# Kernel tuning notes

Hardware: AMD Instinct MI355X
Metric: run time of the kernel (lower is better)

Reference implementation:

```python
import jax, jax.numpy as jnp
import numpy as np
from jax import lax

B_J0 = 0.01   # config.b_j0
R_M = 1.0     # config.R_m
BETA = 1.8    # isAdapt=1 branch
GAMMA = 0.5   # config.gamma
LENS = 0.5    # config.lens
SCALE = 6.0   # config.scale
HIGHT = 0.15  # config.hight


def _gauss(x, mu, sigma):
    return jnp.exp(-(x - mu) ** 2 / (2.0 * sigma ** 2)) / jnp.sqrt(2.0 * jnp.pi) / sigma


@jax.custom_vjp
def spike_fn(x):
    return (x > 0).astype(x.dtype)

def _spike_fwd(x):
    return spike_fn(x), x

def _spike_bwd(x, g):
    # 'MG' multi-gaussian surrogate gradient from ActFun_adp.backward
    temp = (_gauss(x, 0.0, LENS) * (1.0 + HIGHT)
            - _gauss(x, LENS, SCALE * LENS) * HIGHT
            - _gauss(x, -LENS, SCALE * LENS) * HIGHT)
    return (g * temp * GAMMA,)

spike_fn.defvjp(_spike_fwd, _spike_bwd)


def setup_inputs() -> dict:
    key = jax.random.key(0)
    ks = jax.random.split(key, 20)
    B, T, I, H, O = 256, 250, 700, 128, 20
    def xav(k, shape):
        lim = jnp.sqrt(6.0 / (shape[0] + shape[1]))
        return jax.random.uniform(k, shape, jnp.float32, -lim, lim)
    def orth(k, n):
        a = jax.random.normal(k, (n, n), jnp.float32)
        q, r = jnp.linalg.qr(a)
        return q * jnp.sign(jnp.diag(r))[None, :]
    return {
        'input': jax.random.normal(ks[0], (B, T, I), jnp.float32),
        'A1_mask': jnp.ones((H, H), jnp.float32),
        'A2_mask': jnp.ones((H, H), jnp.float32),
        'W_ih1': xav(ks[1], (H, I)), 'b_ih1': jnp.zeros((H,), jnp.float32),
        'W_h1h1': orth(ks[2], H), 'b_h1h1': jnp.zeros((H,), jnp.float32),
        'W_h1h2': xav(ks[3], (H, H)), 'b_h1h2': jnp.zeros((H,), jnp.float32),
        'W_h2h2': orth(ks[4], H), 'b_h2h2': jnp.zeros((H,), jnp.float32),
        'W_h2o': xav(ks[5], (O, H)), 'b_h2o': jnp.zeros((O,), jnp.float32),
        'tau_adp_h1': 150.0 + 10.0 * jax.random.normal(ks[6], (H,), jnp.float32),
        'tau_adp_h2': 150.0 + 10.0 * jax.random.normal(ks[7], (H,), jnp.float32),
        'tau_m_h1': 20.0 + 5.0 * jax.random.normal(ks[8], (H,), jnp.float32),
        'tau_m_h2': 20.0 + 5.0 * jax.random.normal(ks[9], (H,), jnp.float32),
        'tau_m_o': 20.0 + 5.0 * jax.random.normal(ks[10], (O,), jnp.float32),
        'hid1_mem0': jax.random.uniform(ks[11], (B, H), jnp.float32),
        'hid2_mem0': jax.random.uniform(ks[12], (B, H), jnp.float32),
        'out_mem0': jax.random.uniform(ks[13], (B, O), jnp.float32),
    }


def reference(input, A1_mask, A2_mask,
              W_ih1, b_ih1, W_h1h1, b_h1h1, W_h1h2, b_h1h2,
              W_h2h2, b_h2h2, W_h2o, b_h2o,
              tau_adp_h1, tau_adp_h2, tau_m_h1, tau_m_h2, tau_m_o,
              hid1_mem0, hid2_mem0, out_mem0):
    B, T, _ = input.shape
    H = W_ih1.shape[0]
    O = W_h2o.shape[0]
    # time-constant decays (dt = 1), computed once
    a1 = jnp.exp(-1.0 / tau_m_h1)
    r1 = jnp.exp(-1.0 / tau_adp_h1)
    a2 = jnp.exp(-1.0 / tau_m_h2)
    r2 = jnp.exp(-1.0 / tau_adp_h2)
    ao = jnp.exp(-1.0 / tau_m_o)

    xT = jnp.swapaxes(input, 0, 1)  # [T, B, I]
    carry0 = (hid1_mem0, jnp.zeros((B, H), input.dtype), jnp.full((B, H), B_J0, input.dtype),
              hid2_mem0, jnp.zeros((B, H), input.dtype), jnp.full((B, H), B_J0, input.dtype),
              out_mem0, jnp.zeros((B, O), input.dtype))

    def step(carry, xs):
        x_t, t = xs
        h1m, h1s, b1, h2m, h2s, b2, om, acc = carry
        # layer 1: input + recurrent drive, adaptive threshold LIF update
        in1 = x_t @ W_ih1.T + b_ih1 + h1s @ W_h1h1.T + b_h1h1
        b1 = r1 * b1 + (1.0 - r1) * h1s
        Bth1 = B_J0 + BETA * b1
        h1m = h1m * a1 + (1.0 - a1) * R_M * in1 - Bth1 * h1s
        h1s = spike_fn(h1m - Bth1)
        # layer 2
        in2 = h1s @ W_h1h2.T + b_h1h2 + h2s @ W_h2h2.T + b_h2h2
        b2 = r2 * b2 + (1.0 - r2) * h2s
        Bth2 = B_J0 + BETA * b2
        h2m = h2m * a2 + (1.0 - a2) * R_M * in2 - Bth2 * h2s
        h2s = spike_fn(h2m - Bth2)
        # leaky-integrator readout (no spike)
        om = om * ao + (1.0 - ao) * R_M * (h2s @ W_h2o.T + b_h2o)
        # accumulate softmax only for t > 10
        acc = acc + jnp.where(t > 10, 1.0, 0.0) * jax.nn.softmax(om, axis=1)
        return (h1m, h1s, b1, h2m, h2s, b2, om, acc), None

    final, _ = lax.scan(step, carry0, (xT, jnp.arange(T)))
    output = final[-1]
    A_norm = jnp.sum(jnp.abs(W_h1h1)) + jnp.sum(jnp.abs(W_h2h2))
    return output, A_norm


if __name__ == '__main__':
    out = reference(**setup_inputs())
    print(out[0].shape, out[1])
```

## Files before the change

kernel.cpp:

```cpp
#include <hip/hip_runtime.h>
#include <hip/hip_bf16.h>
#include <stdint.h>

#define HN 128
#define TSTEPS 250
#define ON 20
#define GK 700
#define NKT 22

typedef _Float16 h2 __attribute__((ext_vector_type(2)));
typedef _Float16 h8 __attribute__((ext_vector_type(8)));
typedef float f4 __attribute__((ext_vector_type(4)));

__device__ __forceinline__ uint32_t pack2u(float x, float y) {
    h2 p; p.x = (_Float16)x; p.y = (_Float16)y;
    return __builtin_bit_cast(uint32_t, p);
}

__global__ __launch_bounds__(256) void ff_gemm(const float* __restrict__ X,
                                               const float* __restrict__ W,
                                               const float* __restrict__ bias,
                                               float* __restrict__ out) {
    __shared__ __align__(16) uint32_t Xs[2][128][16];
    __shared__ __align__(16) uint32_t Ws[2][128][16];
    const int tid   = threadIdx.x;
    const int w     = tid >> 6;
    const int lane  = tid & 63;
    const int m0    = blockIdx.x * 128;
    const int srow  = tid & 127;
    const int shalf = tid >> 7;
    const int lr    = lane & 15;
    const int lg    = lane >> 4;

    f4 acc[2][8];
#pragma unroll
    for (int m = 0; m < 2; ++m)
#pragma unroll
        for (int n = 0; n < 8; ++n) acc[m][n] = (f4){0.f, 0.f, 0.f, 0.f};

    float4 x4[4], w4[4];

#define LOADT(t)                                                               \
    {                                                                          \
        const int k0 = (t) * 32 + shalf * 16;                                  \
        if ((t) < 21 || shalf == 0) {                                          \
            _Pragma("unroll")                                                  \
            for (int q = 0; q < 4; ++q) {                                      \
                x4[q] = *(const float4*)&X[(size_t)(m0 + srow) * GK + k0 + q * 4]; \
                w4[q] = *(const float4*)&W[(size_t)srow * GK + k0 + q * 4];    \
            }                                                                  \
        } else {                                                               \
            _Pragma("unroll")                                                  \
            for (int q = 0; q < 3; ++q) {                                      \
                x4[q] = *(const float4*)&X[(size_t)(m0 + srow) * GK + k0 + q * 4]; \
                w4[q] = *(const float4*)&W[(size_t)srow * GK + k0 + q * 4];    \
            }                                                                  \
            x4[3] = (float4){0.f, 0.f, 0.f, 0.f};                              \
            w4[3] = (float4){0.f, 0.f, 0.f, 0.f};                              \
        }                                                                      \
    }
#define STORET(buf)                                                            \
    {                                                                          \
        _Pragma("unroll")                                                      \
        for (int q = 0; q < 4; ++q) {                                          \
            Xs[buf][srow][shalf * 8 + 2 * q]     = pack2u(x4[q].x, x4[q].y);   \
            Xs[buf][srow][shalf * 8 + 2 * q + 1] = pack2u(x4[q].z, x4[q].w);   \
            Ws[buf][srow][shalf * 8 + 2 * q]     = pack2u(w4[q].x, w4[q].y);   \
            Ws[buf][srow][shalf * 8 + 2 * q + 1] = pack2u(w4[q].z, w4[q].w);   \
        }                                                                      \
    }

    LOADT(0);
    STORET(0);
    __syncthreads();
    int cur = 0;
    for (int t = 0; t < NKT; ++t) {
        if (t + 1 < NKT) LOADT(t + 1);
        h8 a[2];
#pragma unroll
        for (int m = 0; m < 2; ++m) {
            const uint4 au = *(const uint4*)&Xs[cur][w * 32 + m * 16 + lr][lg * 4];
            a[m] = __builtin_bit_cast(h8, au);
        }
#pragma unroll
        for (int n = 0; n < 8; ++n) {
            const uint4 bu = *(const uint4*)&Ws[cur][n * 16 + lr][lg * 4];
            const h8 bf = __builtin_bit_cast(h8, bu);
            acc[0][n] = __builtin_amdgcn_mfma_f32_16x16x32_f16(a[0], bf, acc[0][n], 0, 0, 0);
            acc[1][n] = __builtin_amdgcn_mfma_f32_16x16x32_f16(a[1], bf, acc[1][n], 0, 0, 0);
        }
        if (t + 1 < NKT) STORET(cur ^ 1);
        __syncthreads();
        cur ^= 1;
    }

    float bv[8];
#pragma unroll
    for (int n = 0; n < 8; ++n) bv[n] = bias[n * 16 + lr];
#pragma unroll
    for (int m = 0; m < 2; ++m)
#pragma unroll
        for (int q = 0; q < 4; ++q) {
            const size_t row = (size_t)(m0 + w * 32 + m * 16 + lg * 4 + q);
#pragma unroll
            for (int n = 0; n < 8; ++n)
                out[row * HN + n * 16 + lr] = acc[m][n][q] + bv[n];
        }
#undef LOADT
#undef STORET
}

__device__ __forceinline__ void qrow(const float* __restrict__ src,
                                     uint4 (&wq)[8], float& sc) {
    float amax = 0.f;
#pragma unroll
    for (int q = 0; q < 32; ++q) {
        float4 v = *(const float4*)&src[q * 4];
        amax = fmaxf(amax, fmaxf(fmaxf(fabsf(v.x), fabsf(v.y)),
                                 fmaxf(fabsf(v.z), fabsf(v.w))));
    }
    const float qs = (amax > 0.f) ? 127.f / amax : 0.f;
#pragma unroll
    for (int g = 0; g < 8; ++g) {
        uint32_t u[4];
#pragma unroll
        for (int e = 0; e < 4; ++e) {
            float4 v = *(const float4*)&src[g * 16 + e * 4];
            const int q0 = (int)rintf(v.x * qs), q1 = (int)rintf(v.y * qs);
            const int q2 = (int)rintf(v.z * qs), q3 = (int)rintf(v.w * qs);
            u[e] = (uint32_t)(q0 & 255) | ((uint32_t)(q1 & 255) << 8) |
                   ((uint32_t)(q2 & 255) << 16) | ((uint32_t)(q3 & 255) << 24);
        }
        wq[g].x = u[0]; wq[g].y = u[1]; wq[g].z = u[2]; wq[g].w = u[3];
    }
    sc = (amax > 0.f) ? amax / 127.f : 0.f;
}

__device__ __forceinline__ int mvqr(const uint4 (&wq)[8], const uint4 (&sv)[8]) {
    int a0 = 0, a1 = 0, a2 = 0, a3 = 0;
#pragma unroll
    for (int g = 0; g < 8; ++g) {
        a0 = __builtin_amdgcn_sdot4((int)wq[g].x, (int)sv[g].x, a0, false);
        a1 = __builtin_amdgcn_sdot4((int)wq[g].y, (int)sv[g].y, a1, false);
        a2 = __builtin_amdgcn_sdot4((int)wq[g].z, (int)sv[g].z, a2, false);
        a3 = __builtin_amdgcn_sdot4((int)wq[g].w, (int)sv[g].w, a3, false);
    }
    return (a0 + a1) + (a2 + a3);
}

#define LOADQ(arr, buf, sv)                                                    \
    {                                                                          \
        const uint4* _p = (const uint4*)&arr[buf][0];                          \
        _Pragma("unroll") for (int _g = 0; _g < 8; ++_g) sv[_g] = _p[_g];      \
    }

__device__ __forceinline__ uint32_t nib2bytes(uint32_t nib) {
    return ((nib & 15u) * 0x00204081u) & 0x01010101u;
}

__device__ __forceinline__ void spread_masks(unsigned long long lo,
                                             unsigned long long hi,
                                             uint4 (&sv)[8]) {
#pragma unroll
    for (int g = 0; g < 8; ++g) {
        const unsigned long long src = (g < 4) ? lo : hi;
        const int base = (g & 3) * 16;
        sv[g].x = nib2bytes((uint32_t)(src >> (base + 0)));
        sv[g].y = nib2bytes((uint32_t)(src >> (base + 4)));
        sv[g].z = nib2bytes((uint32_t)(src >> (base + 8)));
        sv[g].w = nib2bytes((uint32_t)(src >> (base + 12)));
    }
}

#define LDS_FENCE() asm volatile("s_waitcnt lgkmcnt(0)" ::: "memory")

#define PROG_S1 0
#define PROG_B  1
#define PROG_C  2
#define PROG_RO 3
#define PROG_OM 4

__global__ __launch_bounds__(320) void srnn_pipe12(
    const float* __restrict__ ff,
    const float* __restrict__ W_h1h1, const float* __restrict__ b_h1h1,
    const float* __restrict__ W_h1h2, const float* __restrict__ b_h1h2,
    const float* __restrict__ W_h2h2, const float* __restrict__ b_h2h2,
    const float* __restrict__ W_h2o,  const float* __restrict__ b_h2o,
    const float* __restrict__ tau_adp_h1, const float* __restrict__ tau_adp_h2,
    const float* __restrict__ tau_m_h1,   const float* __restrict__ tau_m_h2,
    const float* __restrict__ tau_m_o,
    const float* __restrict__ h1m0, const float* __restrict__ h2m0,
    const float* __restrict__ om0,
    float* __restrict__ out) {
    const int b    = blockIdx.x;
    const int tid  = threadIdx.x;
    const int w    = tid >> 6;
    const int lane = tid & 63;

    __shared__ __align__(16) uint32_t s1ring[8][32];
    __shared__ __align__(16) uint32_t s2ring[8][32];
    __shared__ __align__(16) float    pBring[8][HN];
    __shared__ __align__(16) float    rdring[8][32];
    __shared__ int prog[8];

    if (tid < 8) prog[tid] = 0;
    __syncthreads();

#define WAIT_GE(idx, target, cache)                                            \
    if ((cache) < (target)) {                                                  \
        volatile int* _p = (volatile int*)&prog[idx];                          \
        int _v = *_p;                                                          \
        while (_v < (target)) _v = *_p;                                        \
        (cache) = _v;                                                          \
        LDS_FENCE();                                                           \
    }
#define PUBLISH(idx, val)                                                      \
    {                                                                          \
        LDS_FENCE();                                                           \
        if (lane == 0) ((volatile int*)prog)[idx] = (val);                     \
    }

    if (w == 0) {
        const int jl = lane, jh = lane + 64;
        uint4 wql[8], wqh[8]; float sAl, sAh;
        qrow(W_h1h1 + jl * HN, wql, sAl);
        qrow(W_h1h1 + jh * HN, wqh, sAh);
        float h1m_l = h1m0[b * HN + jl], h1m_h = h1m0[b * HN + jh];
        const float a1l = expf(-1.f / tau_m_h1[jl]), a1h = expf(-1.f / tau_m_h1[jh]);
        const float r1l = expf(-1.f / tau_adp_h1[jl]), r1h = expf(-1.f / tau_adp_h1[jh]);
        const float bil = b_h1h1[jl], bih = b_h1h1[jh];
        float b1l = 0.01f, b1h = 0.01f, s1l = 0.f, s1h = 0.f;
        const float* fpl = ff + (size_t)b * TSTEPS * HN + jl;
        const float* fph = ff + (size_t)b * TSTEPS * HN + jh;
        float fcl = fpl[0], fnl = fpl[HN];
        float fch = fph[0], fnh = fph[HN];
        unsigned long long mklo = 0ull, mkhi = 0ull;
        int cB = 0;
        for (int t = 0; t < TSTEPS; ++t) {
            const float f2l = (t + 2 < TSTEPS) ? fpl[(size_t)(t + 2) * HN] : 0.f;
            const float f2h = (t + 2 < TSTEPS) ? fph[(size_t)(t + 2) * HN] : 0.f;
            uint4 sv[8];
            spread_masks(mklo, mkhi, sv);
            const float pAl = sAl * (float)mvqr(wql, sv);
            const float pAh = sAh * (float)mvqr(wqh, sv);
            b1l = r1l * b1l + (1.f - r1l) * s1l;
            b1h = r1h * b1h + (1.f - r1h) * s1h;
            const float Btl = 0.01f + 1.8f * b1l;
            const float Bth = 0.01f + 1.8f * b1h;
            h1m_l = h1m_l * a1l + (1.f - a1l) * (fcl + bil + pAl) - Btl * s1l;
            h1m_h = h1m_h * a1h + (1.f - a1h) * (fch + bih + pAh) - Bth * s1h;
            const int spl = (h1m_l - Btl > 0.f) ? 1 : 0;
            const int sph = (h1m_h - Bth > 0.f) ? 1 : 0;
            s1l = (float)spl; s1h = (float)sph;
            mklo = __ballot(spl); mkhi = __ballot(sph);
            WAIT_GE(PROG_B, t - 7, cB);
            if (lane < 32) {
                const unsigned long long src = (lane < 16) ? mklo : mkhi;
                s1ring[t & 7][lane] = nib2bytes((uint32_t)(src >> ((lane & 15) * 4)));
            }
            PUBLISH(PROG_S1, t + 1);
            fcl = fnl; fnl = f2l; fch = fnh; fnh = f2h;
        }
    } else if (w == 1) {
        const int jl = lane, jh = lane + 64;
        uint4 wql[8], wqh[8]; float sBl, sBh;
        qrow(W_h1h2 + jl * HN, wql, sBl);
        qrow(W_h1h2 + jh * HN, wqh, sBh);
        int cS1 = 0, cC = 0;
        for (int t = 0; t < TSTEPS; ++t) {
            WAIT_GE(PROG_S1, t + 1, cS1);
            uint4 sv[8];
            LOADQ(s1ring, t & 7, sv);
            const float pl = sBl * (float)mvqr(wql, sv);
            const float ph = sBh * (float)mvqr(wqh, sv);
            WAIT_GE(PROG_C, t - 7, cC);
            pBring[t & 7][jl] = pl;
            pBring[t & 7][jh] = ph;
            PUBLISH(PROG_B, t + 1);
        }
    } else if (w == 2) {
        const int jl = lane, jh = lane + 64;
        uint4 wql[8], wqh[8]; float sCl, sCh;
        qrow(W_h2h2 + jl * HN, wql, sCl);
        qrow(W_h2h2 + jh * HN, wqh, sCh);
        float h2m_l = h2m0[b * HN + jl], h2m_h = h2m0[b * HN + jh];
        const float a2l = expf(-1.f / tau_m_h2[jl]), a2h = expf(-1.f / tau_m_h2[jh]);
        const float r2l = expf(-1.f / tau_adp_h2[jl]), r2h = expf(-1.f / tau_adp_h2[jh]);
        const float bil = b_h1h2[jl] + b_h2h2[jl];
        const float bih = b_h1h2[jh] + b_h2h2[jh];
        float b2l = 0.01f, b2h = 0.01f, s2l = 0.f, s2h = 0.f;
        unsigned long long mklo = 0ull, mkhi = 0ull;
        int cB = 0, cRO = 0;
        for (int t = 0; t < TSTEPS; ++t) {
            uint4 sv[8];
            spread_masks(mklo, mkhi, sv);
            const float pCl = sCl * (float)mvqr(wql, sv);
            const float pCh = sCh * (float)mvqr(wqh, sv);
            WAIT_GE(PROG_B, t + 1, cB);
            const float pBl = pBring[t & 7][jl];
            const float pBh = pBring[t & 7][jh];
            b2l = r2l * b2l + (1.f - r2l) * s2l;
            b2h = r2h * b2h + (1.f - r2h) * s2h;
            const float Btl = 0.01f + 1.8f * b2l;
            const float Bth = 0.01f + 1.8f * b2h;
            h2m_l = h2m_l * a2l + (1.f - a2l) * (pBl + pCl + bil) - Btl * s2l;
            h2m_h = h2m_h * a2h + (1.f - a2h) * (pBh + pCh + bih) - Bth * s2h;
            const int spl = (h2m_l - Btl > 0.f) ? 1 : 0;
            const int sph = (h2m_h - Bth > 0.f) ? 1 : 0;
            s2l = (float)spl; s2h = (float)sph;
            mklo = __ballot(spl); mkhi = __ballot(sph);
            WAIT_GE(PROG_RO, t - 7, cRO);
            if (lane < 32) {
                const unsigned long long src = (lane < 16) ? mklo : mkhi;
                s2ring[t & 7][lane] = nib2bytes((uint32_t)(src >> ((lane & 15) * 4)));
            }
            PUBLISH(PROG_C, t + 1);
        }
    } else if (w == 3) {
        const int o = lane;
        uint4 wq[8]; float sO;
        qrow(W_h2o + (size_t)((o < ON) ? o : 0) * HN, wq, sO);
        if (o >= ON) sO = 0.f;
        int cC = 0, cOM = 0;
        for (int t = 0; t < TSTEPS; ++t) {
            WAIT_GE(PROG_C, t + 1, cC);
            uint4 sv[8];
            LOADQ(s2ring, t & 7, sv);
            const float r = sO * (float)mvqr(wq, sv);
            WAIT_GE(PROG_OM, t - 7, cOM);
            if (o < 32) rdring[t & 7][o] = (o < ON) ? r : 0.f;
            PUBLISH(PROG_RO, t + 1);
        }
    } else {
        float omv[ON], accv[ON], aov[ON], bov[ON];
#pragma unroll
        for (int k = 0; k < ON; ++k) {
            omv[k]  = om0[b * ON + k];
            aov[k]  = expf(-1.f / tau_m_o[k]);
            bov[k]  = b_h2o[k];
            accv[k] = 0.f;
        }
        int cRO = 0;
        for (int t = 0; t < TSTEPS; ++t) {
            WAIT_GE(PROG_RO, t + 1, cRO);
            const float4* rp = (const float4*)&rdring[t & 7][0];
            const float4 r0 = rp[0], r1 = rp[1], r2 = rp[2], r3 = rp[3], r4 = rp[4];
            float rd[ON];
            rd[0] = r0.x;  rd[1] = r0.y;  rd[2] = r0.z;  rd[3] = r0.w;
            rd[4] = r1.x;  rd[5] = r1.y;  rd[6] = r1.z;  rd[7] = r1.w;
            rd[8] = r2.x;  rd[9] = r2.y;  rd[10] = r2.z; rd[11] = r2.w;
            rd[12] = r3.x; rd[13] = r3.y; rd[14] = r3.z; rd[15] = r3.w;
            rd[16] = r4.x; rd[17] = r4.y; rd[18] = r4.z; rd[19] = r4.w;
            PUBLISH(PROG_OM, t + 1);
#pragma unroll
            for (int k = 0; k < ON; ++k)
                omv[k] = omv[k] * aov[k] + (1.f - aov[k]) * (rd[k] + bov[k]);
            float m0 = omv[0], m1 = omv[1], m2 = omv[2], m3 = omv[3];
#pragma unroll
            for (int k = 4; k < ON; k += 4) {
                m0 = fmaxf(m0, omv[k]);
                m1 = fmaxf(m1, omv[k + 1]);
                m2 = fmaxf(m2, omv[k + 2]);
                m3 = fmaxf(m3, omv[k + 3]);
            }
            const float mx = fmaxf(fmaxf(m0, m1), fmaxf(m2, m3));
            float e[ON];
            float d0 = 0.f, d1 = 0.f, d2 = 0.f, d3 = 0.f;
#pragma unroll
            for (int k = 0; k < ON; k += 4) {
                e[k]     = __expf(omv[k] - mx);     d0 += e[k];
                e[k + 1] = __expf(omv[k + 1] - mx); d1 += e[k + 1];
                e[k + 2] = __expf(omv[k + 2] - mx); d2 += e[k + 2];
                e[k + 3] = __expf(omv[k + 3] - mx); d3 += e[k + 3];
            }
            const float den = (d0 + d1) + (d2 + d3);
            if (t > 10) {
                const float rden = 1.f / den;
#pragma unroll
                for (int k = 0; k < ON; ++k)
                    accv[k] = fmaf(e[k], rden, accv[k]);
            }
        }
        if (lane == 0) {
#pragma unroll
            for (int k = 0; k < ON; ++k) out[b * ON + k] = accv[k];
        }
    }
#undef WAIT_GE
#undef PUBLISH
}

__global__ void anorm_kernel(const float* __restrict__ W1,
                             const float* __restrict__ W2,
                             float* __restrict__ out) {
    __shared__ float red[256];
    float s = 0.f;
    for (int i = threadIdx.x; i < HN * HN; i += 256)
        s += fabsf(W1[i]) + fabsf(W2[i]);
    red[threadIdx.x] = s;
    __syncthreads();
    for (int off = 128; off > 0; off >>= 1) {
        if (threadIdx.x < off) red[threadIdx.x] += red[threadIdx.x + off];
        __syncthreads();
    }
    if (threadIdx.x == 0) out[256 * ON] = red[0];
}

extern "C" void kernel_launch(void* const* d_in, const int* in_sizes, int n_in,
                              void* d_out, int out_size, void* d_ws, size_t ws_size,
                              hipStream_t stream) {
    const float* input      = (const float*)d_in[0];
    const float* W_ih1      = (const float*)d_in[3];
    const float* b_ih1      = (const float*)d_in[4];
    const float* W_h1h1     = (const float*)d_in[5];
    const float* b_h1h1     = (const float*)d_in[6];
    const float* W_h1h2     = (const float*)d_in[7];
    const float* b_h1h2     = (const float*)d_in[8];
    const float* W_h2h2     = (const float*)d_in[9];
    const float* b_h2h2     = (const float*)d_in[10];
    const float* W_h2o      = (const float*)d_in[11];
    const float* b_h2o      = (const float*)d_in[12];
    const float* tau_adp_h1 = (const float*)d_in[13];
    const float* tau_adp_h2 = (const float*)d_in[14];
    const float* tau_m_h1   = (const float*)d_in[15];
    const float* tau_m_h2   = (const float*)d_in[16];
    const float* tau_m_o    = (const float*)d_in[17];
    const float* h1m0       = (const float*)d_in[18];
    const float* h2m0       = (const float*)d_in[19];
    const float* om0        = (const float*)d_in[20];

    float* out   = (float*)d_out;
    float* ffbuf = (float*)d_ws;

    anorm_kernel<<<1, 256, 0, stream>>>(W_h1h1, W_h2h2, out);
    ff_gemm<<<500, 256, 0, stream>>>(input, W_ih1, b_ih1, ffbuf);
    srnn_pipe12<<<256, 320, 0, stream>>>(ffbuf, W_h1h1, b_h1h1, W_h1h2, b_h1h2,
                                         W_h2h2, b_h2h2, W_h2o, b_h2o,
                                         tau_adp_h1, tau_adp_h2,
                                         tau_m_h1, tau_m_h2, tau_m_o,
                                         h1m0, h2m0, om0, out);
}
```

Baseline: 239.2 us.

## Replace per-step LDS spin-wait flags with chunked barrier-synchronized wavefront pipeline

```diff
diff --git a/kernel.cpp b/kernel.cpp
--- a/kernel.cpp
+++ b/kernel.cpp
@@ -7,6 +7,8 @@
 #define ON 20
 #define GK 700
 #define NKT 22
+#define KS 4
+#define NSLOT 63
 
 typedef _Float16 h2 __attribute__((ext_vector_type(2)));
 typedef _Float16 h8 __attribute__((ext_vector_type(8)));
@@ -148,9 +150,9 @@
     return (a0 + a1) + (a2 + a3);
 }
 
-#define LOADQ(arr, buf, sv)                                                    \
+#define LOADQP(ptr, sv)                                                        \
     {                                                                          \
-        const uint4* _p = (const uint4*)&arr[buf][0];                          \
+        const uint4* _p = (const uint4*)(ptr);                                 \
         _Pragma("unroll") for (int _g = 0; _g < 8; ++_g) sv[_g] = _p[_g];      \
     }
 
@@ -172,15 +174,7 @@
     }
 }
 
-#define LDS_FENCE() asm volatile("s_waitcnt lgkmcnt(0)" ::: "memory")
-
-#define PROG_S1 0
-#define PROG_B  1
-#define PROG_C  2
-#define PROG_RO 3
-#define PROG_OM 4
-
-__global__ __launch_bounds__(320) void srnn_pipe12(
+__global__ __launch_bounds__(320) void srnn_pipe13(
     const float* __restrict__ ff,
     const float* __restrict__ W_h1h1, const float* __restrict__ b_h1h1,
     const float* __restrict__ W_h1h2, const float* __restrict__ b_h1h2,
@@ -197,28 +191,10 @@
     const int w    = tid >> 6;
     const int lane = tid & 63;
 
-    __shared__ __align__(16) uint32_t s1ring[8][32];
-    __shared__ __align__(16) uint32_t s2ring[8][32];
-    __shared__ __align__(16) float    pBring[8][HN];
-    __shared__ __align__(16) float    rdring[8][32];
-    __shared__ int prog[8];
-
-    if (tid < 8) prog[tid] = 0;
-    __syncthreads();
-
-#define WAIT_GE(idx, target, cache)                                            \
-    if ((cache) < (target)) {                                                  \
-        volatile int* _p = (volatile int*)&prog[idx];                          \
-        int _v = *_p;                                                          \
-        while (_v < (target)) _v = *_p;                                        \
-        (cache) = _v;                                                          \
-        LDS_FENCE();                                                           \
-    }
-#define PUBLISH(idx, val)                                                      \
-    {                                                                          \
-        LDS_FENCE();                                                           \
-        if (lane == 0) ((volatile int*)prog)[idx] = (val);                     \
-    }
+    __shared__ __align__(16) uint32_t s1buf[2][KS][32];
+    __shared__ __align__(16) uint32_t s2buf[2][KS][32];
+    __shared__ __align__(16) float    pbbuf[2][KS][HN];
+    __shared__ __align__(16) float    rdbuf[2][KS][32];
 
     if (w == 0) {
         const int jl = lane, jh = lane + 64;
@@ -232,51 +208,71 @@
         float b1l = 0.01f, b1h = 0.01f, s1l = 0.f, s1h = 0.f;
         const float* fpl = ff + (size_t)b * TSTEPS * HN + jl;
         const float* fph = ff + (size_t)b * TSTEPS * HN + jh;
-        float fcl = fpl[0], fnl = fpl[HN];
-        float fch = fph[0], fnh = fph[HN];
+        float fcl[KS], fch[KS];
+#pragma unroll
+        for (int k = 0; k < KS; ++k) {
+            fcl[k] = fpl[(size_t)k * HN];
+            fch[k] = fph[(size_t)k * HN];
+        }
         unsigned long long mklo = 0ull, mkhi = 0ull;
-        int cB = 0;
-        for (int t = 0; t < TSTEPS; ++t) {
-            const float f2l = (t + 2 < TSTEPS) ? fpl[(size_t)(t + 2) * HN] : 0.f;
-            const float f2h = (t + 2 < TSTEPS) ? fph[(size_t)(t + 2) * HN] : 0.f;
-            uint4 sv[8];
-            spread_masks(mklo, mkhi, sv);
-            const float pAl = sAl * (float)mvqr(wql, sv);
-            const float pAh = sAh * (float)mvqr(wqh, sv);
-            b1l = r1l * b1l + (1.f - r1l) * s1l;
-            b1h = r1h * b1h + (1.f - r1h) * s1h;
-            const float Btl = 0.01f + 1.8f * b1l;
-            const float Bth = 0.01f + 1.8f * b1h;
-            h1m_l = h1m_l * a1l + (1.f - a1l) * (fcl + bil + pAl) - Btl * s1l;
-            h1m_h = h1m_h * a1h + (1.f - a1h) * (fch + bih + pAh) - Bth * s1h;
-            const int spl = (h1m_l - Btl > 0.f) ? 1 : 0;
-            const int sph = (h1m_h - Bth > 0.f) ? 1 : 0;
-            s1l = (float)spl; s1h = (float)sph;
-            mklo = __ballot(spl); mkhi = __ballot(sph);
-            WAIT_GE(PROG_B, t - 7, cB);
-            if (lane < 32) {
-                const unsigned long long src = (lane < 16) ? mklo : mkhi;
-                s1ring[t & 7][lane] = nib2bytes((uint32_t)(src >> ((lane & 15) * 4)));
-            }
-            PUBLISH(PROG_S1, t + 1);
-            fcl = fnl; fnl = f2l; fch = fnh; fnh = f2h;
+        for (int s = 0; s < NSLOT + 4; ++s) {
+            float fnl[KS], fnh[KS];
+#pragma unroll
+            for (int k = 0; k < KS; ++k) {
+                const int t = KS * (s + 1) + k;
+                fnl[k] = (t < TSTEPS) ? fpl[(size_t)t * HN] : 0.f;
+                fnh[k] = (t < TSTEPS) ? fph[(size_t)t * HN] : 0.f;
+            }
+            if (s < NSLOT) {
+#pragma unroll
+                for (int k = 0; k < KS; ++k) {
+                    const int t = KS * s + k;
+                    if (t < TSTEPS) {
+                        uint4 sv[8];
+                        spread_masks(mklo, mkhi, sv);
+                        const float pAl = sAl * (float)mvqr(wql, sv);
+                        const float pAh = sAh * (float)mvqr(wqh, sv);
+                        b1l = r1l * b1l + (1.f - r1l) * s1l;
+                        b1h = r1h * b1h + (1.f - r1h) * s1h;
+                        const float Btl = 0.01f + 1.8f * b1l;
+                        const float Bth = 0.01f + 1.8f * b1h;
+                        h1m_l = h1m_l * a1l + (1.f - a1l) * (fcl[k] + bil + pAl) - Btl * s1l;
+                        h1m_h = h1m_h * a1h + (1.f - a1h) * (fch[k] + bih + pAh) - Bth * s1h;
+                        const int spl = (h1m_l - Btl > 0.f) ? 1 : 0;
+                        const int sph = (h1m_h - Bth > 0.f) ? 1 : 0;
+                        s1l = (float)spl; s1h = (float)sph;
+                        mklo = __ballot(spl); mkhi = __ballot(sph);
+                        if (lane < 32) {
+                            const unsigned long long src = (lane < 16) ? mklo : mkhi;
+                            s1buf[s & 1][k][lane] =
+                                nib2bytes((uint32_t)(src >> ((lane & 15) * 4)));
+                        }
+                    }
+                }
+            }
+#pragma unroll
+            for (int k = 0; k < KS; ++k) { fcl[k] = fnl[k]; fch[k] = fnh[k]; }
+            __syncthreads();
         }
     } else if (w == 1) {
         const int jl = lane, jh = lane + 64;
         uint4 wql[8], wqh[8]; float sBl, sBh;
         qrow(W_h1h2 + jl * HN, wql, sBl);
         qrow(W_h1h2 + jh * HN, wqh, sBh);
-        int cS1 = 0, cC = 0;
-        for (int t = 0; t < TSTEPS; ++t) {
-            WAIT_GE(PROG_S1, t + 1, cS1);
-            uint4 sv[8];
-            LOADQ(s1ring, t & 7, sv);
-            const float pl = sBl * (float)mvqr(wql, sv);
-            const float ph = sBh * (float)mvqr(wqh, sv);
-            WAIT_GE(PROG_C, t - 7, cC);
-            pBring[t & 7][jl] = pl;
-            pBring[t & 7][jh] = ph;
-            PUBLISH(PROG_B, t + 1);
+        for (int s = 0; s < NSLOT + 4; ++s) {
+            if (s >= 1 && s - 1 < NSLOT) {
+#pragma unroll
+                for (int k = 0; k < KS; ++k) {
+                    const int t = KS * (s - 1) + k;
+                    if (t < TSTEPS) {
+                        uint4 sv[8];
+                        LOADQP(&s1buf[(s - 1) & 1][k][0], sv);
+                        pbbuf[s & 1][k][jl] = sBl * (float)mvqr(wql, sv);
+                        pbbuf[s & 1][k][jh] = sBh * (float)mvqr(wqh, sv);
+                    }
+                }
+            }
+            __syncthreads();
         }
     } else if (w == 2) {
         const int jl = lane, jh = lane + 64;
@@ -290,46 +286,56 @@
         const float bih = b_h1h2[jh] + b_h2h2[jh];
         float b2l = 0.01f, b2h = 0.01f, s2l = 0.f, s2h = 0.f;
         unsigned long long mklo = 0ull, mkhi = 0ull;
-        int cB = 0, cRO = 0;
-        for (int t = 0; t < TSTEPS; ++t) {
-            uint4 sv[8];
-            spread_masks(mklo, mkhi, sv);
-            const float pCl = sCl * (float)mvqr(wql, sv);
-            const float pCh = sCh * (float)mvqr(wqh, sv);
-            WAIT_GE(PROG_B, t + 1, cB);
-            const float pBl = pBring[t & 7][jl];
-            const float pBh = pBring[t & 7][jh];
-            b2l = r2l * b2l + (1.f - r2l) * s2l;
-            b2h = r2h * b2h + (1.f - r2h) * s2h;
-            const float Btl = 0.01f + 1.8f * b2l;
-            const float Bth = 0.01f + 1.8f * b2h;
-            h2m_l = h2m_l * a2l + (1.f - a2l) * (pBl + pCl + bil) - Btl * s2l;
-            h2m_h = h2m_h * a2h + (1.f - a2h) * (pBh + pCh + bih) - Bth * s2h;
-            const int spl = (h2m_l - Btl > 0.f) ? 1 : 0;
-            const int sph = (h2m_h - Bth > 0.f) ? 1 : 0;
-            s2l = (float)spl; s2h = (float)sph;
-            mklo = __ballot(spl); mkhi = __ballot(sph);
-            WAIT_GE(PROG_RO, t - 7, cRO);
-            if (lane < 32) {
-                const unsigned long long src = (lane < 16) ? mklo : mkhi;
-                s2ring[t & 7][lane] = nib2bytes((uint32_t)(src >> ((lane & 15) * 4)));
-            }
-            PUBLISH(PROG_C, t + 1);
+        for (int s = 0; s < NSLOT + 4; ++s) {
+            if (s >= 2 && s - 2 < NSLOT) {
+#pragma unroll
+                for (int k = 0; k < KS; ++k) {
+                    const int t = KS * (s - 2) + k;
+                    if (t < TSTEPS) {
+                        uint4 sv[8];
+                        spread_masks(mklo, mkhi, sv);
+                        const float pCl = sCl * (float)mvqr(wql, sv);
+                        const float pCh = sCh * (float)mvqr(wqh, sv);
+                        const float pBl = pbbuf[(s - 1) & 1][k][jl];
+                        const float pBh = pbbuf[(s - 1) & 1][k][jh];
+                        b2l = r2l * b2l + (1.f - r2l) * s2l;
+                        b2h = r2h * b2h + (1.f - r2h) * s2h;
+                        const float Btl = 0.01f + 1.8f * b2l;
+                        const float Bth = 0.01f + 1.8f * b2h;
+                        h2m_l = h2m_l * a2l + (1.f - a2l) * (pBl + pCl + bil) - Btl * s2l;
+                        h2m_h = h2m_h * a2h + (1.f - a2h) * (pBh + pCh + bih) - Bth * s2h;
+                        const int spl = (h2m_l - Btl > 0.f) ? 1 : 0;
+                        const int sph = (h2m_h - Bth > 0.f) ? 1 : 0;
+                        s2l = (float)spl; s2h = (float)sph;
+                        mklo = __ballot(spl); mkhi = __ballot(sph);
+                        if (lane < 32) {
+                            const unsigned long long src = (lane < 16) ? mklo : mkhi;
+                            s2buf[s & 1][k][lane] =
+                                nib2bytes((uint32_t)(src >> ((lane & 15) * 4)));
+                        }
+                    }
+                }
+            }
+            __syncthreads();
         }
     } else if (w == 3) {
         const int o = lane;
         uint4 wq[8]; float sO;
         qrow(W_h2o + (size_t)((o < ON) ? o : 0) * HN, wq, sO);
         if (o >= ON) sO = 0.f;
-        int cC = 0, cOM = 0;
-        for (int t = 0; t < TSTEPS; ++t) {
-            WAIT_GE(PROG_C, t + 1, cC);
-            uint4 sv[8];
-            LOADQ(s2ring, t & 7, sv);
-            const float r = sO * (float)mvqr(wq, sv);
-            WAIT_GE(PROG_OM, t - 7, cOM);
-            if (o < 32) rdring[t & 7][o] = (o < ON) ? r : 0.f;
-            PUBLISH(PROG_RO, t + 1);
+        for (int s = 0; s < NSLOT + 4; ++s) {
+            if (s >= 3 && s - 3 < NSLOT) {
+#pragma unroll
+                for (int k = 0; k < KS; ++k) {
+                    const int t = KS * (s - 3) + k;
+                    if (t < TSTEPS) {
+                        uint4 sv[8];
+                        LOADQP(&s2buf[(s - 1) & 1][k][0], sv);
+                        if (o < 32) rdbuf[s & 1][k][o] = sO * (float)mvqr(wq, sv);
+                    }
+                }
+            }
+            __syncthreads();
         }
     } else {
         float omv[ON], accv[ON], aov[ON], bov[ON];
@@ -340,54 +346,59 @@
             bov[k]  = b_h2o[k];
             accv[k] = 0.f;
         }
-        int cRO = 0;
-        for (int t = 0; t < TSTEPS; ++t) {
-            WAIT_GE(PROG_RO, t + 1, cRO);
-            const float4* rp = (const float4*)&rdring[t & 7][0];
-            const float4 r0 = rp[0], r1 = rp[1], r2 = rp[2], r3 = rp[3], r4 = rp[4];
-            float rd[ON];
-            rd[0] = r0.x;  rd[1] = r0.y;  rd[2] = r0.z;  rd[3] = r0.w;
-            rd[4] = r1.x;  rd[5] = r1.y;  rd[6] = r1.z;  rd[7] = r1.w;
-            rd[8] = r2.x;  rd[9] = r2.y;  rd[10] = r2.z; rd[11] = r2.w;
-            rd[12] = r3.x; rd[13] = r3.y; rd[14] = r3.z; rd[15] = r3.w;
-            rd[16] = r4.x; rd[17] = r4.y; rd[18] = r4.z; rd[19] = r4.w;
-            PUBLISH(PROG_OM, t + 1);
-#pragma unroll
-            for (int k = 0; k < ON; ++k)
-                omv[k] = omv[k] * aov[k] + (1.f - aov[k]) * (rd[k] + bov[k]);
-            float m0 = omv[0], m1 = omv[1], m2 = omv[2], m3 = omv[3];
-#pragma unroll
-            for (int k = 4; k < ON; k += 4) {
-                m0 = fmaxf(m0, omv[k]);
-                m1 = fmaxf(m1, omv[k + 1]);
-                m2 = fmaxf(m2, omv[k + 2]);
-                m3 = fmaxf(m3, omv[k + 3]);
-            }
-            const float mx = fmaxf(fmaxf(m0, m1), fmaxf(m2, m3));
-            float e[ON];
-            float d0 = 0.f, d1 = 0.f, d2 = 0.f, d3 = 0.f;
-#pragma unroll
-            for (int k = 0; k < ON; k += 4) {
-                e[k]     = __expf(omv[k] - mx);     d0 += e[k];
-                e[k + 1] = __expf(omv[k + 1] - mx); d1 += e[k + 1];
-                e[k + 2] = __expf(omv[k + 2] - mx); d2 += e[k + 2];
-                e[k + 3] = __expf(omv[k + 3] - mx); d3 += e[k + 3];
-            }
-            const float den = (d0 + d1) + (d2 + d3);
-            if (t > 10) {
-                const float rden = 1.f / den;
-#pragma unroll
-                for (int k = 0; k < ON; ++k)
-                    accv[k] = fmaf(e[k], rden, accv[k]);
-            }
+        for (int s = 0; s < NSLOT + 4; ++s) {
+            if (s >= 4 && s - 4 < NSLOT) {
+#pragma unroll
+                for (int kk = 0; kk < KS; ++kk) {
+                    const int t = KS * (s - 4) + kk;
+                    if (t < TSTEPS) {
+                        const float4* rp = (const float4*)&rdbuf[(s - 1) & 1][kk][0];
+                        const float4 r0 = rp[0], r1 = rp[1], r2 = rp[2],
+                                     r3 = rp[3], r4 = rp[4];
+                        float rd[ON];
+                        rd[0] = r0.x;  rd[1] = r0.y;  rd[2] = r0.z;  rd[3] = r0.w;
+                        rd[4] = r1.x;  rd[5] = r1.y;  rd[6] = r1.z;  rd[7] = r1.w;
+                        rd[8] = r2.x;  rd[9] = r2.y;  rd[10] = r2.z; rd[11] = r2.w;
+                        rd[12] = r3.x; rd[13] = r3.y; rd[14] = r3.z; rd[15] = r3.w;
+                        rd[16] = r4.x; rd[17] = r4.y; rd[18] = r4.z; rd[19] = r4.w;
+#pragma unroll
+                        for (int k = 0; k < ON; ++k)
+                            omv[k] = omv[k] * aov[k] + (1.f - aov[k]) * (rd[k] + bov[k]);
+                        float m0 = omv[0], m1 = omv[1], m2 = omv[2], m3 = omv[3];
+#pragma unroll
+                        for (int k = 4; k < ON; k += 4) {
+                            m0 = fmaxf(m0, omv[k]);
+                            m1 = fmaxf(m1, omv[k + 1]);
+                            m2 = fmaxf(m2, omv[k + 2]);
+                            m3 = fmaxf(m3, omv[k + 3]);
+                        }
+                        const float mx = fmaxf(fmaxf(m0, m1), fmaxf(m2, m3));
+                        float e[ON];
+                        float d0 = 0.f, d1 = 0.f, d2 = 0.f, d3 = 0.f;
+#pragma unroll
+                        for (int k = 0; k < ON; k += 4) {
+                            e[k]     = __expf(omv[k] - mx);     d0 += e[k];
+                            e[k + 1] = __expf(omv[k + 1] - mx); d1 += e[k + 1];
+                            e[k + 2] = __expf(omv[k + 2] - mx); d2 += e[k + 2];
+                            e[k + 3] = __expf(omv[k + 3] - mx); d3 += e[k + 3];
+                        }
+                        const float den = (d0 + d1) + (d2 + d3);
+                        if (t > 10) {
+                            const float rden = 1.f / den;
+#pragma unroll
+                            for (int k = 0; k < ON; ++k)
+                                accv[k] = fmaf(e[k], rden, accv[k]);
+                        }
+                    }
+                }
+            }
+            __syncthreads();
         }
         if (lane == 0) {
 #pragma unroll
             for (int k = 0; k < ON; ++k) out[b * ON + k] = accv[k];
         }
     }
-#undef WAIT_GE
-#undef PUBLISH
 }
 
 __global__ void anorm_kernel(const float* __restrict__ W1,
@@ -434,7 +445,7 @@
 
     anorm_kernel<<<1, 256, 0, stream>>>(W_h1h1, W_h2h2, out);
     ff_gemm<<<500, 256, 0, stream>>>(input, W_ih1, b_ih1, ffbuf);
-    srnn_pipe12<<<256, 320, 0, stream>>>(ffbuf, W_h1h1, b_h1h1, W_h1h2, b_h1h2,
+    srnn_pipe13<<<256, 320, 0, stream>>>(ffbuf, W_h1h1, b_h1h1, W_h1h2, b_h1h2,
                                          W_h2h2, b_h2h2, W_h2o, b_h2o,
                                          tau_adp_h1, tau_adp_h2,
                                          tau_m_h1, tau_m_h2, tau_m_o,
```

New measurement: 247.1 us. 1.03x slower.

## Collapse five-wave pipelined SRNN kernel into single-wave monolithic recurrence

Applied to the files above, without the earlier changes.

```diff
diff --git a/kernel.cpp b/kernel.cpp
--- a/kernel.cpp
+++ b/kernel.cpp
@@ -110,8 +110,13 @@
 #undef STORET
 }
 
-__device__ __forceinline__ void qrow(const float* __restrict__ src,
-                                     uint4 (&wq)[8], float& sc) {
+__device__ __forceinline__ float rlane(float v, int k) {
+    return __int_as_float(__builtin_amdgcn_readlane(__float_as_int(v), k));
+}
+
+template <int STRIDE>
+__device__ __forceinline__ void qrow_lds(const float* __restrict__ src,
+                                         uint4 (*WQ)[STRIDE], int j, float& sc) {
     float amax = 0.f;
 #pragma unroll
     for (int q = 0; q < 32; ++q) {
@@ -131,28 +136,26 @@
             u[e] = (uint32_t)(q0 & 255) | ((uint32_t)(q1 & 255) << 8) |
                    ((uint32_t)(q2 & 255) << 16) | ((uint32_t)(q3 & 255) << 24);
         }
-        wq[g].x = u[0]; wq[g].y = u[1]; wq[g].z = u[2]; wq[g].w = u[3];
+        uint4 w4; w4.x = u[0]; w4.y = u[1]; w4.z = u[2]; w4.w = u[3];
+        WQ[g][j] = w4;
     }
     sc = (amax > 0.f) ? amax / 127.f : 0.f;
 }
 
-__device__ __forceinline__ int mvqr(const uint4 (&wq)[8], const uint4 (&sv)[8]) {
+template <int STRIDE>
+__device__ __forceinline__ int mvql(const uint4 (*W)[STRIDE],
+                                    const uint4 (&sv)[8], int j) {
     int a0 = 0, a1 = 0, a2 = 0, a3 = 0;
 #pragma unroll
     for (int g = 0; g < 8; ++g) {
-        a0 = __builtin_amdgcn_sdot4((int)wq[g].x, (int)sv[g].x, a0, false);
-        a1 = __builtin_amdgcn_sdot4((int)wq[g].y, (int)sv[g].y, a1, false);
-        a2 = __builtin_amdgcn_sdot4((int)wq[g].z, (int)sv[g].z, a2, false);
-        a3 = __builtin_amdgcn_sdot4((int)wq[g].w, (int)sv[g].w, a3, false);
+        const uint4 wq = W[g][j];
+        a0 = __builtin_amdgcn_sdot4((int)wq.x, (int)sv[g].x, a0, false);
+        a1 = __builtin_amdgcn_sdot4((int)wq.y, (int)sv[g].y, a1, false);
+        a2 = __builtin_amdgcn_sdot4((int)wq.z, (int)sv[g].z, a2, false);
+        a3 = __builtin_amdgcn_sdot4((int)wq.w, (int)sv[g].w, a3, false);
     }
     return (a0 + a1) + (a2 + a3);
 }
-
-#define LOADQ(arr, buf, sv)                                                    \
-    {                                                                          \
-        const uint4* _p = (const uint4*)&arr[buf][0];                          \
-        _Pragma("unroll") for (int _g = 0; _g < 8; ++_g) sv[_g] = _p[_g];      \
-    }
 
 __device__ __forceinline__ uint32_t nib2bytes(uint32_t nib) {
     return ((nib & 15u) * 0x00204081u) & 0x01010101u;
@@ -172,15 +175,7 @@
     }
 }
 
-#define LDS_FENCE() asm volatile("s_waitcnt lgkmcnt(0)" ::: "memory")
-
-#define PROG_S1 0
-#define PROG_B  1
-#define PROG_C  2
-#define PROG_RO 3
-#define PROG_OM 4
-
-__global__ __launch_bounds__(320) void srnn_pipe12(
+__global__ __launch_bounds__(64) void srnn_mono(
     const float* __restrict__ ff,
     const float* __restrict__ W_h1h1, const float* __restrict__ b_h1h1,
     const float* __restrict__ W_h1h2, const float* __restrict__ b_h1h2,
@@ -193,201 +188,115 @@
     const float* __restrict__ om0,
     float* __restrict__ out) {
     const int b    = blockIdx.x;
-    const int tid  = threadIdx.x;
-    const int w    = tid >> 6;
-    const int lane = tid & 63;
-
-    __shared__ __align__(16) uint32_t s1ring[8][32];
-    __shared__ __align__(16) uint32_t s2ring[8][32];
-    __shared__ __align__(16) float    pBring[8][HN];
-    __shared__ __align__(16) float    rdring[8][32];
-    __shared__ int prog[8];
-
-    if (tid < 8) prog[tid] = 0;
+    const int lane = threadIdx.x;
+    const int jl = lane, jh = lane + 64;
+
+    __shared__ __align__(16) uint4 WQA[8][HN];
+    __shared__ __align__(16) uint4 WQB[8][HN];
+    __shared__ __align__(16) uint4 WQC[8][HN];
+    __shared__ __align__(16) uint4 WQO[8][64];
+
+    float sAl, sAh, sBl, sBh, sCl, sCh, sO;
+    qrow_lds<HN>(W_h1h1 + jl * HN, WQA, jl, sAl);
+    qrow_lds<HN>(W_h1h1 + jh * HN, WQA, jh, sAh);
+    qrow_lds<HN>(W_h1h2 + jl * HN, WQB, jl, sBl);
+    qrow_lds<HN>(W_h1h2 + jh * HN, WQB, jh, sBh);
+    qrow_lds<HN>(W_h2h2 + jl * HN, WQC, jl, sCl);
+    qrow_lds<HN>(W_h2h2 + jh * HN, WQC, jh, sCh);
+    qrow_lds<64>(W_h2o + (size_t)((lane < ON) ? lane : 0) * HN, WQO, lane, sO);
+    if (lane >= ON) sO = 0.f;
     __syncthreads();
 
-#define WAIT_GE(idx, target, cache)                                            \
-    if ((cache) < (target)) {                                                  \
-        volatile int* _p = (volatile int*)&prog[idx];                          \
-        int _v = *_p;                                                          \
-        while (_v < (target)) _v = *_p;                                        \
-        (cache) = _v;                                                          \
-        LDS_FENCE();                                                           \
-    }
-#define PUBLISH(idx, val)                                                      \
-    {                                                                          \
-        LDS_FENCE();                                                           \
-        if (lane == 0) ((volatile int*)prog)[idx] = (val);                     \
-    }
-
-    if (w == 0) {
-        const int jl = lane, jh = lane + 64;
-        uint4 wql[8], wqh[8]; float sAl, sAh;
-        qrow(W_h1h1 + jl * HN, wql, sAl);
-        qrow(W_h1h1 + jh * HN, wqh, sAh);
-        float h1m_l = h1m0[b * HN + jl], h1m_h = h1m0[b * HN + jh];
-        const float a1l = expf(-1.f / tau_m_h1[jl]), a1h = expf(-1.f / tau_m_h1[jh]);
-        const float r1l = expf(-1.f / tau_adp_h1[jl]), r1h = expf(-1.f / tau_adp_h1[jh]);
-        const float bil = b_h1h1[jl], bih = b_h1h1[jh];
-        float b1l = 0.01f, b1h = 0.01f, s1l = 0.f, s1h = 0.f;
-        const float* fpl = ff + (size_t)b * TSTEPS * HN + jl;
-        const float* fph = ff + (size_t)b * TSTEPS * HN + jh;
-        float fcl = fpl[0], fnl = fpl[HN];
-        float fch = fph[0], fnh = fph[HN];
-        unsigned long long mklo = 0ull, mkhi = 0ull;
-        int cB = 0;
-        for (int t = 0; t < TSTEPS; ++t) {
-            const float f2l = (t + 2 < TSTEPS) ? fpl[(size_t)(t + 2) * HN] : 0.f;
-            const float f2h = (t + 2 < TSTEPS) ? fph[(size_t)(t + 2) * HN] : 0.f;
-            uint4 sv[8];
-            spread_masks(mklo, mkhi, sv);
-            const float pAl = sAl * (float)mvqr(wql, sv);
-            const float pAh = sAh * (float)mvqr(wqh, sv);
-            b1l = r1l * b1l + (1.f - r1l) * s1l;
-            b1h = r1h * b1h + (1.f - r1h) * s1h;
-            const float Btl = 0.01f + 1.8f * b1l;
-            const float Bth = 0.01f + 1.8f * b1h;
-            h1m_l = h1m_l * a1l + (1.f - a1l) * (fcl + bil + pAl) - Btl * s1l;
-            h1m_h = h1m_h * a1h + (1.f - a1h) * (fch + bih + pAh) - Bth * s1h;
-            const int spl = (h1m_l - Btl > 0.f) ? 1 : 0;
-            const int sph = (h1m_h - Bth > 0.f) ? 1 : 0;
-            s1l = (float)spl; s1h = (float)sph;
-            mklo = __ballot(spl); mkhi = __ballot(sph);
-            WAIT_GE(PROG_B, t - 7, cB);
-            if (lane < 32) {
-                const unsigned long long src = (lane < 16) ? mklo : mkhi;
-                s1ring[t & 7][lane] = nib2bytes((uint32_t)(src >> ((lane & 15) * 4)));
-            }
-            PUBLISH(PROG_S1, t + 1);
-            fcl = fnl; fnl = f2l; fch = fnh; fnh = f2h;
-        }
-    } else if (w == 1) {
-        const int jl = lane, jh = lane + 64;
-        uint4 wql[8], wqh[8]; float sBl, sBh;
-        qrow(W_h1h2 + jl * HN, wql, sBl);
-        qrow(W_h1h2 + jh * HN, wqh, sBh);
-        int cS1 = 0, cC = 0;
-        for (int t = 0; t < TSTEPS; ++t) {
-            WAIT_GE(PROG_S1, t + 1, cS1);
-            uint4 sv[8];
-            LOADQ(s1ring, t & 7, sv);
-            const float pl = sBl * (float)mvqr(wql, sv);
-            const float ph = sBh * (float)mvqr(wqh, sv);
-            WAIT_GE(PROG_C, t - 7, cC);
-            pBring[t & 7][jl] = pl;
-            pBring[t & 7][jh] = ph;
-            PUBLISH(PROG_B, t + 1);
-        }
-    } else if (w == 2) {
-        const int jl = lane, jh = lane + 64;
-        uint4 wql[8], wqh[8]; float sCl, sCh;
-        qrow(W_h2h2 + jl * HN, wql, sCl);
-        qrow(W_h2h2 + jh * HN, wqh, sCh);
-        float h2m_l = h2m0[b * HN + jl], h2m_h = h2m0[b * HN + jh];
-        const float a2l = expf(-1.f / tau_m_h2[jl]), a2h = expf(-1.f / tau_m_h2[jh]);
-        const float r2l = expf(-1.f / tau_adp_h2[jl]), r2h = expf(-1.f / tau_adp_h2[jh]);
-        const float bil = b_h1h2[jl] + b_h2h2[jl];
-        const float bih = b_h1h2[jh] + b_h2h2[jh];
-        float b2l = 0.01f, b2h = 0.01f, s2l = 0.f, s2h = 0.f;
-        unsigned long long mklo = 0ull, mkhi = 0ull;
-        int cB = 0, cRO = 0;
-        for (int t = 0; t < TSTEPS; ++t) {
-            uint4 sv[8];
-            spread_masks(mklo, mkhi, sv);
-            const float pCl = sCl * (float)mvqr(wql, sv);
-            const float pCh = sCh * (float)mvqr(wqh, sv);
-            WAIT_GE(PROG_B, t + 1, cB);
-            const float pBl = pBring[t & 7][jl];
-            const float pBh = pBring[t & 7][jh];
-            b2l = r2l * b2l + (1.f - r2l) * s2l;
-            b2h = r2h * b2h + (1.f - r2h) * s2h;
-            const float Btl = 0.01f + 1.8f * b2l;
-            const float Bth = 0.01f + 1.8f * b2h;
-            h2m_l = h2m_l * a2l + (1.f - a2l) * (pBl + pCl + bil) - Btl * s2l;
-            h2m_h = h2m_h * a2h + (1.f - a2h) * (pBh + pCh + bih) - Bth * s2h;
-            const int spl = (h2m_l - Btl > 0.f) ? 1 : 0;
-            const int sph = (h2m_h - Bth > 0.f) ? 1 : 0;
-            s2l = (float)spl; s2h = (float)sph;
-            mklo = __ballot(spl); mkhi = __ballot(sph);
-            WAIT_GE(PROG_RO, t - 7, cRO);
-            if (lane < 32) {
-                const unsigned long long src = (lane < 16) ? mklo : mkhi;
-                s2ring[t & 7][lane] = nib2bytes((uint32_t)(src >> ((lane & 15) * 4)));
-            }
-            PUBLISH(PROG_C, t + 1);
-        }
-    } else if (w == 3) {
-        const int o = lane;
-        uint4 wq[8]; float sO;
-        qrow(W_h2o + (size_t)((o < ON) ? o : 0) * HN, wq, sO);
-        if (o >= ON) sO = 0.f;
-        int cC = 0, cOM = 0;
-        for (int t = 0; t < TSTEPS; ++t) {
-            WAIT_GE(PROG_C, t + 1, cC);
-            uint4 sv[8];
-            LOADQ(s2ring, t & 7, sv);
-            const float r = sO * (float)mvqr(wq, sv);
-            WAIT_GE(PROG_OM, t - 7, cOM);
-            if (o < 32) rdring[t & 7][o] = (o < ON) ? r : 0.f;
-            PUBLISH(PROG_RO, t + 1);
-        }
-    } else {
-        float omv[ON], accv[ON], aov[ON], bov[ON];
-#pragma unroll
-        for (int k = 0; k < ON; ++k) {
-            omv[k]  = om0[b * ON + k];
-            aov[k]  = expf(-1.f / tau_m_o[k]);
-            bov[k]  = b_h2o[k];
-            accv[k] = 0.f;
-        }
-        int cRO = 0;
-        for (int t = 0; t < TSTEPS; ++t) {
-            WAIT_GE(PROG_RO, t + 1, cRO);
-            const float4* rp = (const float4*)&rdring[t & 7][0];
-            const float4 r0 = rp[0], r1 = rp[1], r2 = rp[2], r3 = rp[3], r4 = rp[4];
-            float rd[ON];
-            rd[0] = r0.x;  rd[1] = r0.y;  rd[2] = r0.z;  rd[3] = r0.w;
-            rd[4] = r1.x;  rd[5] = r1.y;  rd[6] = r1.z;  rd[7] = r1.w;
-            rd[8] = r2.x;  rd[9] = r2.y;  rd[10] = r2.z; rd[11] = r2.w;
-            rd[12] = r3.x; rd[13] = r3.y; rd[14] = r3.z; rd[15] = r3.w;
-            rd[16] = r4.x; rd[17] = r4.y; rd[18] = r4.z; rd[19] = r4.w;
-            PUBLISH(PROG_OM, t + 1);
-#pragma unroll
-            for (int k = 0; k < ON; ++k)
-                omv[k] = omv[k] * aov[k] + (1.f - aov[k]) * (rd[k] + bov[k]);
-            float m0 = omv[0], m1 = omv[1], m2 = omv[2], m3 = omv[3];
+    float h1m_l = h1m0[b * HN + jl], h1m_h = h1m0[b * HN + jh];
+    const float a1l = expf(-1.f / tau_m_h1[jl]), a1h = expf(-1.f / tau_m_h1[jh]);
+    const float r1l = expf(-1.f / tau_adp_h1[jl]), r1h = expf(-1.f / tau_adp_h1[jh]);
+    const float bi1l = b_h1h1[jl], bi1h = b_h1h1[jh];
+    float h2m_l = h2m0[b * HN + jl], h2m_h = h2m0[b * HN + jh];
+    const float a2l = expf(-1.f / tau_m_h2[jl]), a2h = expf(-1.f / tau_m_h2[jh]);
+    const float r2l = expf(-1.f / tau_adp_h2[jl]), r2h = expf(-1.f / tau_adp_h2[jh]);
+    const float bi2l = b_h1h2[jl] + b_h2h2[jl];
+    const float bi2h = b_h1h2[jh] + b_h2h2[jh];
+    float b1l = 0.01f, b1h = 0.01f, s1l = 0.f, s1h = 0.f;
+    float b2l = 0.01f, b2h = 0.01f, s2l = 0.f, s2h = 0.f;
+    float om = 0.f, ao = 0.f, bo = 0.f, acc = 0.f;
+    if (lane < ON) {
+        om = om0[b * ON + lane];
+        ao = expf(-1.f / tau_m_o[lane]);
+        bo = b_h2o[lane];
+    }
+
+    const float* fpl = ff + (size_t)b * TSTEPS * HN + jl;
+    const float* fph = ff + (size_t)b * TSTEPS * HN + jh;
+    float fcl = fpl[0], fnl = fpl[HN];
+    float fch = fph[0], fnh = fph[HN];
+
+    uint4 sv1[8], sv2[8];
+    spread_masks(0ull, 0ull, sv1);
+    spread_masks(0ull, 0ull, sv2);
+
+    for (int t = 0; t < TSTEPS; ++t) {
+        const float f2l = (t + 2 < TSTEPS) ? fpl[(size_t)(t + 2) * HN] : 0.f;
+        const float f2h = (t + 2 < TSTEPS) ? fph[(size_t)(t + 2) * HN] : 0.f;
+
+        const float pAl = sAl * (float)mvql<HN>(WQA, sv1, jl);
+        const float pAh = sAh * (float)mvql<HN>(WQA, sv1, jh);
+        b1l = r1l * b1l + (1.f - r1l) * s1l;
+        b1h = r1h * b1h + (1.f - r1h) * s1h;
+        const float Bt1l = 0.01f + 1.8f * b1l;
+        const float Bt1h = 0.01f + 1.8f * b1h;
+        h1m_l = h1m_l * a1l + (1.f - a1l) * (fcl + bi1l + pAl) - Bt1l * s1l;
+        h1m_h = h1m_h * a1h + (1.f - a1h) * (fch + bi1h + pAh) - Bt1h * s1h;
+        const int sp1l = (h1m_l - Bt1l > 0.f) ? 1 : 0;
+        const int sp1h = (h1m_h - Bt1h > 0.f) ? 1 : 0;
+        s1l = (float)sp1l; s1h = (float)sp1h;
+        spread_masks(__ballot(sp1l), __ballot(sp1h), sv1);
+
+        const float pBl = sBl * (float)mvql<HN>(WQB, sv1, jl);
+        const float pBh = sBh * (float)mvql<HN>(WQB, sv1, jh);
+        const float pCl = sCl * (float)mvql<HN>(WQC, sv2, jl);
+        const float pCh = sCh * (float)mvql<HN>(WQC, sv2, jh);
+        b2l = r2l * b2l + (1.f - r2l) * s2l;
+        b2h = r2h * b2h + (1.f - r2h) * s2h;
+        const float Bt2l = 0.01f + 1.8f * b2l;
+        const float Bt2h = 0.01f + 1.8f * b2h;
+        h2m_l = h2m_l * a2l + (1.f - a2l) * (pBl + pCl + bi2l) - Bt2l * s2l;
+        h2m_h = h2m_h * a2h + (1.f - a2h) * (pBh + pCh + bi2h) - Bt2h * s2h;
+        const int sp2l = (h2m_l - Bt2l > 0.f) ? 1 : 0;
+        const int sp2h = (h2m_h - Bt2h > 0.f) ? 1 : 0;
+        s2l = (float)sp2l; s2h = (float)sp2h;
+        spread_masks(__ballot(sp2l), __ballot(sp2h), sv2);
+
+        const float rdot = sO * (float)mvql<64>(WQO, sv2, lane);
+
+        om = om * ao + (1.f - ao) * (rdot + bo);
+        if (t > 10) {
+            float omk[ON];
+#pragma unroll
+            for (int k = 0; k < ON; ++k) omk[k] = rlane(om, k);
+            float m0 = omk[0], m1 = omk[1], m2 = omk[2], m3 = omk[3];
 #pragma unroll
             for (int k = 4; k < ON; k += 4) {
-                m0 = fmaxf(m0, omv[k]);
-                m1 = fmaxf(m1, omv[k + 1]);
-                m2 = fmaxf(m2, omv[k + 2]);
-                m3 = fmaxf(m3, omv[k + 3]);
+                m0 = fmaxf(m0, omk[k]);
+                m1 = fmaxf(m1, omk[k + 1]);
+                m2 = fmaxf(m2, omk[k + 2]);
+                m3 = fmaxf(m3, omk[k + 3]);
             }
             const float mx = fmaxf(fmaxf(m0, m1), fmaxf(m2, m3));
-            float e[ON];
             float d0 = 0.f, d1 = 0.f, d2 = 0.f, d3 = 0.f;
 #pragma unroll
             for (int k = 0; k < ON; k += 4) {
-                e[k]     = __expf(omv[k] - mx);     d0 += e[k];
-                e[k + 1] = __expf(omv[k + 1] - mx); d1 += e[k + 1];
-                e[k + 2] = __expf(omv[k + 2] - mx); d2 += e[k + 2];
-                e[k + 3] = __expf(omv[k + 3] - mx); d3 += e[k + 3];
+                d0 += __expf(omk[k] - mx);
+                d1 += __expf(omk[k + 1] - mx);
+                d2 += __expf(omk[k + 2] - mx);
+                d3 += __expf(omk[k + 3] - mx);
             }
             const float den = (d0 + d1) + (d2 + d3);
-            if (t > 10) {
-                const float rden = 1.f / den;
-#pragma unroll
-                for (int k = 0; k < ON; ++k)
-                    accv[k] = fmaf(e[k], rden, accv[k]);
-            }
-        }
-        if (lane == 0) {
-#pragma unroll
-            for (int k = 0; k < ON; ++k) out[b * ON + k] = accv[k];
-        }
-    }
-#undef WAIT_GE
-#undef PUBLISH
+            acc += __expf(om - mx) / den;
+        }
+        fcl = fnl; fnl = f2l; fch = fnh; fnh = f2h;
+    }
+
+    if (lane < ON) out[b * ON + lane] = acc;
 }
 
 __global__ void anorm_kernel(const float* __restrict__ W1,
@@ -434,9 +343,9 @@
 
     anorm_kernel<<<1, 256, 0, stream>>>(W_h1h1, W_h2h2, out);
     ff_gemm<<<500, 256, 0, stream>>>(input, W_ih1, b_ih1, ffbuf);
-    srnn_pipe12<<<256, 320, 0, stream>>>(ffbuf, W_h1h1, b_h1h1, W_h1h2, b_h1h2,
-                                         W_h2h2, b_h2h2, W_h2o, b_h2o,
-                                         tau_adp_h1, tau_adp_h2,
-                                         tau_m_h1, tau_m_h2, tau_m_o,
-                                         h1m0, h2m0, om0, out);
-}
+    srnn_mono<<<256, 64, 0, stream>>>(ffbuf, W_h1h1, b_h1h1, W_h1h2, b_h1h2,
+                                      W_h2h2, b_h2h2, W_h2o, b_h2o,
+                                      tau_adp_h1, tau_adp_h2,
+                                      tau_m_h1, tau_m_h2, tau_m_o,
+                                      h1m0, h2m0, om0, out);
+}
```

Result: slower. 434.1 us (+81.5%).
